# Kernel tuning notes

Hardware: AMD Instinct MI355X
Metric: run time of the kernel (lower is better)

## Reference

```python
import jax, jax.numpy as jnp
import numpy as np

N = 100000   # nodes
E = 3200000  # edges
G = 256      # graphs in batch
C_IN, H, OUT = 5, 64, 2
EPS = 1e-5


def setup_inputs() -> dict:
    key = jax.random.key(0)
    ks = jax.random.split(key, 16)
    d = {
        "x": jax.random.normal(ks[0], (N, C_IN), jnp.float32),
        "edge_index": jax.random.randint(ks[1], (2, E), 0, N, jnp.int64),
        "batch": jnp.sort(jax.random.randint(ks[2], (N,), 0, G, jnp.int64)),
        "W1": jax.random.normal(ks[3], (C_IN, H), jnp.float32),
        "b1": jax.random.normal(ks[4], (H,), jnp.float32),
        "g1": jax.random.uniform(ks[5], (H,), jnp.float32),
        "be1": jax.random.normal(ks[6], (H,), jnp.float32),
        "rm1": jnp.zeros((H,), jnp.float32),
        "rv1": jnp.ones((H,), jnp.float32),
        "W2": jax.random.normal(ks[7], (H, H), jnp.float32),
        "b2": jax.random.normal(ks[8], (H,), jnp.float32),
        "g2": jax.random.uniform(ks[9], (H,), jnp.float32),
        "be2": jax.random.normal(ks[10], (H,), jnp.float32),
        "rm2": jnp.zeros((H,), jnp.float32),
        "rv2": jnp.ones((H,), jnp.float32),
        "W3": jax.random.normal(ks[11], (H, H), jnp.float32),
        "b3": jax.random.normal(ks[12], (H,), jnp.float32),
        "g3": jax.random.uniform(ks[13], (H,), jnp.float32),
        "be3": jax.random.normal(ks[14], (H,), jnp.float32),
        "rm3": jnp.zeros((H,), jnp.float32),
        "rv3": jnp.ones((H,), jnp.float32),
        "Wf1": jax.random.normal(ks[15], (H, 32), jnp.float32),
        "bf1": jax.random.normal(jax.random.fold_in(key, 1), (32,), jnp.float32),
        "Wf2": jax.random.normal(jax.random.fold_in(key, 2), (32, OUT), jnp.float32),
        "bf2": jax.random.normal(jax.random.fold_in(key, 3), (OUT,), jnp.float32),
    }
    return d


def reference(x, edge_index, batch, W1, b1, g1, be1, rm1, rv1,
              W2, b2, g2, be2, rm2, rv2, W3, b3, g3, be3, rm3, rv3,
              Wf1, bf1, Wf2, bf2):
    src, dst = edge_index[0], edge_index[1]
    # GCN symmetric normalization with self-loops: deg includes the self edge
    deg = jax.ops.segment_sum(jnp.ones((E,), x.dtype), dst, num_segments=N) + 1.0
    dinv = jax.lax.rsqrt(deg)            # [N]
    enorm = dinv[src] * dinv[dst]        # per-edge norm  [E]
    snorm = dinv * dinv                  # self-loop norm [N]

    def gcn(h, W, b):
        h = h @ W                                                  # [N,H]
        agg = jax.ops.segment_sum(h[src] * enorm[:, None], dst, num_segments=N)
        return agg + h * snorm[:, None] + b

    def bn(h, g, be, rm, rv):  # eval-mode BatchNorm1d
        return (h - rm) * jax.lax.rsqrt(rv + EPS) * g + be

    h = jax.nn.relu(bn(gcn(x, W1, b1), g1, be1, rm1, rv1))
    h = jax.nn.relu(bn(gcn(h, W2, b2), g2, be2, rm2, rv2))
    h = jax.nn.relu(bn(gcn(h, W3, b3), g3, be3, rm3, rv3))

    counts = jax.ops.segment_sum(jnp.ones((N,), h.dtype), batch, num_segments=G)
    pooled = jax.ops.segment_sum(h, batch, num_segments=G) / jnp.maximum(counts, 1.0)[:, None]

    h = jax.nn.relu(pooled @ Wf1 + bf1)  # dropout is identity in eval
    return jax.nn.sigmoid(h @ Wf2 + bf2)
```

## Files before the change

### kernel.cpp

```cpp
#include <hip/hip_runtime.h>
#include <hip/hip_bf16.h>

#define HF 64
#define EPS 1e-5f

#define BSH 9
#define BKN (1 << BSH)
#define NBUCK_MAX 256
#define PB_T 256
#define PB_EPT 32
#define PB_TILE (PB_T * PB_EPT)

#define LGRID 2048

typedef __hip_bfloat16 bf16;

__device__ __forceinline__ unsigned char f32_to_fp8(float v) {
    int p = __builtin_amdgcn_cvt_pk_fp8_f32(v, v, 0, false);
    return (unsigned char)(p & 0xff);
}

__device__ __forceinline__ float rdlane(float v, int k) {
    return __int_as_float(__builtin_amdgcn_readlane(__float_as_int(v), k));
}

__device__ __forceinline__ unsigned bf16_rne_hi(float x) {
    unsigned u = __float_as_uint(x);
    return (u + 0x7fffu + ((u >> 16) & 1u)) & 0xffff0000u;
}

__global__ __launch_bounds__(PB_T) void k_passB2(
    const int* __restrict__ src, const int* __restrict__ dst,
    int* __restrict__ stage, unsigned* __restrict__ rtab,
    int* __restrict__ bcnt, int E, int B) {
    __shared__ int scnt[NBUCK_MAX];
    __shared__ int sscan[PB_T];
    int t = threadIdx.x;
    int blk = blockIdx.x;
    int tile0 = blk * PB_TILE;

    for (int b = t; b < NBUCK_MAX; b += PB_T) scnt[b] = 0;
    __syncthreads();

    int rec[PB_EPT];
    int bkt[PB_EPT];
#pragma unroll
    for (int k = 0; k < PB_EPT; ++k) {
        int e = tile0 + k * PB_T + t;
        bkt[k] = -1;
        if (e < E) {
            int d = dst[e];
            int s = src[e];
            int b = d >> BSH;
            bkt[k] = b;
            rec[k] = s | ((d & (BKN - 1)) << 17);
            atomicAdd(&scnt[b], 1);
        }
    }
    __syncthreads();

    int v = (t < B) ? scnt[t] : 0;
    sscan[t] = v;
    __syncthreads();
    for (int off = 1; off < PB_T; off <<= 1) {
        int val = sscan[t];
        int add = (t >= off) ? sscan[t - off] : 0;
        __syncthreads();
        sscan[t] = val + add;
        __syncthreads();
    }
    int excl = sscan[t] - v;
    if (t < B) {
        rtab[(size_t)blk * B + t] = ((unsigned)excl << 14) | (unsigned)v;
        scnt[t] = excl;
        if (v) atomicAdd(&bcnt[t], v);
    }
    __syncthreads();

#pragma unroll
    for (int k = 0; k < PB_EPT; ++k) {
        if (bkt[k] >= 0) {
            int loc = atomicAdd(&scnt[bkt[k]], 1);
            stage[tile0 + loc] = rec[k];
        }
    }
}

__global__ void k_bscan3(const int* __restrict__ bcnt, int* __restrict__ bbase2,
                         int* __restrict__ base, int B, int N, int E) {
    __shared__ int tot[NBUCK_MAX];
    int t = threadIdx.x;
    int v = (t < B) ? bcnt[t] : 0;
    tot[t] = v;
    __syncthreads();
    for (int off = 1; off < 256; off <<= 1) {
        int val = tot[t];
        int add = (t >= off) ? tot[t - off] : 0;
        __syncthreads();
        tot[t] = val + add;
        __syncthreads();
    }
    if (t < B) bbase2[t] = tot[t] - v;
    if (t == 0) { bbase2[B] = E; base[N] = E; }
}

__global__ __launch_bounds__(512) void k_passC2(const int* __restrict__ stage,
                                                const unsigned* __restrict__ rtab,
                                                const int* __restrict__ bb2,
                                                int* __restrict__ base,
                                                float* __restrict__ dinv,
                                                int* __restrict__ csr,
                                                int N, int B, int nblk) {
    __shared__ int lcnt[BKN];
    __shared__ int lscan[BKN];
    __shared__ int lcur[BKN];
    int beta = blockIdx.x;
    int n0 = beta * BKN;
    int n1 = n0 + BKN; if (n1 > N) n1 = N;
    int nn = n1 - n0;
    int t = threadIdx.x;
    int rg = t >> 4;
    int le = t & 15;
    lcnt[t] = 0;
    __syncthreads();

    for (int blk0 = 0; blk0 < nblk; blk0 += 32) {
        int blk = blk0 + rg;
        if (blk < nblk) {
            unsigned rt = rtab[(size_t)blk * B + beta];
            int cnt = (int)(rt & 0x3FFFu);
            int off = blk * PB_TILE + (int)(rt >> 14);
            for (int i = le; i < cnt; i += 16)
                atomicAdd(&lcnt[stage[off + i] >> 17], 1);
        }
    }
    __syncthreads();
    int v = lcnt[t];
    lscan[t] = v;
    __syncthreads();
    for (int off = 1; off < 512; off <<= 1) {
        int val = lscan[t];
        int add = (t >= off) ? lscan[t - off] : 0;
        __syncthreads();
        lscan[t] = val + add;
        __syncthreads();
    }
    int b = bb2[beta] + lscan[t] - v;
    if (t < nn) {
        base[n0 + t] = b;
        dinv[n0 + t] = rsqrtf((float)v + 1.0f);
    }
    lcur[t] = b;
    __syncthreads();

    for (int blk0 = 0; blk0 < nblk; blk0 += 32) {
        int blk = blk0 + rg;
        if (blk < nblk) {
            unsigned rt = rtab[(size_t)blk * B + beta];
            int cnt = (int)(rt & 0x3FFFu);
            int off = blk * PB_TILE + (int)(rt >> 14);
            for (int i = le; i < cnt; i += 16) {
                int r = stage[off + i];
                int pos = atomicAdd(&lcur[r >> 17], 1);
                csr[pos] = r & 0x1ffff;
            }
        }
    }
}

__global__ void k_prescale(const float* __restrict__ x, const float* __restrict__ dinv,
                           float* __restrict__ xs, int N5) {
    int i = blockIdx.x * blockDim.x + threadIdx.x;
    if (i < N5) xs[i] = x[i] * dinv[i / 5];
}

__global__ __launch_bounds__(256) void k_layer1(
    const float* __restrict__ xs, unsigned char* __restrict__ hout,
    const int* __restrict__ csr, const int* __restrict__ basep,
    const float* __restrict__ dinv,
    const float* __restrict__ W1, const float* __restrict__ b,
    const float* __restrict__ g, const float* __restrict__ be,
    const float* __restrict__ rm, const float* __restrict__ rv, int N) {
    __shared__ float sW[5 * HF];
    __shared__ float sB[HF];
    __shared__ float sScale[HF];
    if (threadIdx.x < HF) {
        int f = threadIdx.x;
        float scale = g[f] * rsqrtf(rv[f] + EPS);
        sScale[f] = scale;
        sB[f] = (b[f] - rm[f]) * scale + be[f];
    }
    __syncthreads();
    for (int i = threadIdx.x; i < 5 * HF; i += blockDim.x)
        sW[i] = W1[i] * sScale[i & (HF - 1)];
    __syncthreads();

    int lane = threadIdx.x & 63;
    int wave = threadIdx.x >> 6;
    int c  = lane & 7;
    int g8 = lane >> 3;
    int stride = gridDim.x * 4;

    auto mlp_store = [&](float accS, int nodeS, float diS) {
        float out = sB[lane];
#pragma unroll
        for (int k = 0; k < 5; ++k) out += __shfl(accS, k, 64) * sW[k * HF + lane];
        out = fmaxf(out, 0.f);
        hout[(size_t)nodeS * HF + lane] = f32_to_fp8(out * diS);
    };

    float accP = 0.f, diP = 0.f;
    int nodeP = -1;

    for (int node = blockIdx.x * 4 + wave; node < N; node += stride) {
        int j   = __builtin_amdgcn_readfirstlane(basep[node]);
        int end = __builtin_amdgcn_readfirstlane(basep[node + 1]);

        float a0 = 0.f, a1 = 0.f, a2 = 0.f, a3 = 0.f;
        if (g8 == 0 && c < 5) a0 = xs[node * 5 + c];

        float u0 = 0.f, u1 = 0.f, u2 = 0.f, u3 = 0.f;
        bool w0 = (j + 32 <= end);
        if (w0) {
            int s0 = csr[j + g8];
            int s1 = csr[j + 8 + g8];
            int s2 = csr[j + 16 + g8];
            int s3 = csr[j + 24 + g8];
            u0 = xs[s0 * 5 + c]; u1 = xs[s1 * 5 + c];
            u2 = xs[s2 * 5 + c]; u3 = xs[s3 * 5 + c];
        }

        if (nodeP >= 0) mlp_store(accP, nodeP, diP);

        if (w0) {
            j += 32;
            while (j + 32 <= end) {
                int s0 = csr[j + g8];
                int s1 = csr[j + 8 + g8];
                int s2 = csr[j + 16 + g8];
                int s3 = csr[j + 24 + g8];
                float v0 = xs[s0 * 5 + c];
                float v1 = xs[s1 * 5 + c];
                float v2 = xs[s2 * 5 + c];
                float v3 = xs[s3 * 5 + c];
                a0 += u0; a1 += u1; a2 += u2; a3 += u3;
                u0 = v0; u1 = v1; u2 = v2; u3 = v3;
                j += 32;
            }
            a0 += u0; a1 += u1; a2 += u2; a3 += u3;
        }
        for (; j + 8 <= end; j += 8) {
            int s = csr[j + g8];
            a0 += xs[s * 5 + c];
        }
        if (j < end && j + g8 < end) {
            int s = csr[j + g8];
            a0 += xs[s * 5 + c];
        }

        float acc = (a0 + a1) + (a2 + a3);
        acc += __shfl_xor(acc, 8, 64);
        acc += __shfl_xor(acc, 16, 64);
        acc += __shfl_xor(acc, 32, 64);

        float di = dinv[node];
        accP = acc * di;
        diP = di;
        nodeP = node;
    }
    if (nodeP >= 0) mlp_store(accP, nodeP, diP);
}

template <int SCALE_OUT>
__global__ __launch_bounds__(256, 4) void k_layer(
    const unsigned char* __restrict__ hs8, void* __restrict__ hout_v,
    const int* __restrict__ csr, const int* __restrict__ basep,
    const float* __restrict__ dinv,
    const float* __restrict__ W, const float* __restrict__ b,
    const float* __restrict__ g, const float* __restrict__ be,
    const float* __restrict__ rm, const float* __restrict__ rv, int N) {
    __shared__ uint4 swp4[64][9];

    int lane = threadIdx.x & 63;
    int wave = threadIdx.x >> 6;
    int stride = gridDim.x * 4;
    const unsigned char* col = hs8 + lane;

    if (threadIdx.x < 64) {
        int l = threadIdx.x;
        float sc = g[l] * rsqrtf(rv[l] + EPS);
#pragma unroll
        for (int c = 0; c < 8; ++c) {
            unsigned p[4];
#pragma unroll
            for (int q = 0; q < 4; ++q) {
                int k2 = c * 4 + q;
                unsigned lo = bf16_rne_hi(W[(2 * k2 + 0) * HF + l] * sc);
                unsigned hi = bf16_rne_hi(W[(2 * k2 + 1) * HF + l] * sc);
                p[q] = (lo >> 16) | hi;
            }
            swp4[l][c] = make_uint4(p[0], p[1], p[2], p[3]);
        }
    }
    __syncthreads();

    float scale = g[lane] * rsqrtf(rv[lane] + EPS);
    float bias  = (b[lane] - rm[lane]) * scale + be[lane];

    auto mlp_store = [&](float acc, int nodeS, float diS) {
        float o0 = bias, o1 = 0.f, o2 = 0.f, o3 = 0.f;
#pragma unroll
        for (int c = 0; c < 8; ++c) {
            uint4 pv = swp4[lane][c];
            int k0 = c * 8;
            o0 += rdlane(acc, k0 + 0) * __uint_as_float(pv.x << 16);
            o1 += rdlane(acc, k0 + 1) * __uint_as_float(pv.x & 0xffff0000u);
            o2 += rdlane(acc, k0 + 2) * __uint_as_float(pv.y << 16);
            o3 += rdlane(acc, k0 + 3) * __uint_as_float(pv.y & 0xffff0000u);
            o0 += rdlane(acc, k0 + 4) * __uint_as_float(pv.z << 16);
            o1 += rdlane(acc, k0 + 5) * __uint_as_float(pv.z & 0xffff0000u);
            o2 += rdlane(acc, k0 + 6) * __uint_as_float(pv.w << 16);
            o3 += rdlane(acc, k0 + 7) * __uint_as_float(pv.w & 0xffff0000u);
        }
        float out = fmaxf((o0 + o1) + (o2 + o3), 0.f);
        if (SCALE_OUT) {
            ((unsigned char*)hout_v)[(size_t)nodeS * HF + lane] = f32_to_fp8(out * diS);
        } else {
            ((float*)hout_v)[(size_t)nodeS * HF + lane] = out;
        }
    };

    float accP = 0.f, diP = 0.f;
    int nodeP = -1;

    for (int node = blockIdx.x * 4 + wave; node < N; node += stride) {
        int j   = __builtin_amdgcn_readfirstlane(basep[node]);
        int end = __builtin_amdgcn_readfirstlane(basep[node + 1]);

        float a0 = __builtin_amdgcn_cvt_f32_fp8((unsigned)col[(size_t)node * HF], 0);
        float a1 = 0.f, a2 = 0.f, a3 = 0.f;

        unsigned u0 = 0, u1 = 0, u2 = 0, u3 = 0, u4 = 0, u5 = 0, u6 = 0, u7 = 0;
        bool w0 = (j + 8 <= end);
        if (w0) {
            int s0 = csr[j+0], s1 = csr[j+1], s2 = csr[j+2], s3 = csr[j+3];
            int s4 = csr[j+4], s5 = csr[j+5], s6 = csr[j+6], s7 = csr[j+7];
            u0 = col[(size_t)s0 * HF]; u1 = col[(size_t)s1 * HF];
            u2 = col[(size_t)s2 * HF]; u3 = col[(size_t)s3 * HF];
            u4 = col[(size_t)s4 * HF]; u5 = col[(size_t)s5 * HF];
            u6 = col[(size_t)s6 * HF]; u7 = col[(size_t)s7 * HF];
        }

        if (nodeP >= 0) mlp_store(accP, nodeP, diP);

        if (w0) {
            j += 8;
            while (j + 8 <= end) {
                int t0 = csr[j+0], t1 = csr[j+1], t2 = csr[j+2], t3 = csr[j+3];
                int t4 = csr[j+4], t5 = csr[j+5], t6 = csr[j+6], t7 = csr[j+7];
                unsigned v0 = col[(size_t)t0 * HF];
                unsigned v1 = col[(size_t)t1 * HF];
                unsigned v2 = col[(size_t)t2 * HF];
                unsigned v3 = col[(size_t)t3 * HF];
                unsigned v4 = col[(size_t)t4 * HF];
                unsigned v5 = col[(size_t)t5 * HF];
                unsigned v6 = col[(size_t)t6 * HF];
                unsigned v7 = col[(size_t)t7 * HF];
                a0 += __builtin_amdgcn_cvt_f32_fp8(u0, 0);
                a1 += __builtin_amdgcn_cvt_f32_fp8(u1, 0);
                a2 += __builtin_amdgcn_cvt_f32_fp8(u2, 0);
                a3 += __builtin_amdgcn_cvt_f32_fp8(u3, 0);
                a0 += __builtin_amdgcn_cvt_f32_fp8(u4, 0);
                a1 += __builtin_amdgcn_cvt_f32_fp8(u5, 0);
                a2 += __builtin_amdgcn_cvt_f32_fp8(u6, 0);
                a3 += __builtin_amdgcn_cvt_f32_fp8(u7, 0);
                u0 = v0; u1 = v1; u2 = v2; u3 = v3;
                u4 = v4; u5 = v5; u6 = v6; u7 = v7;
                j += 8;
            }
            a0 += __builtin_amdgcn_cvt_f32_fp8(u0, 0);
            a1 += __builtin_amdgcn_cvt_f32_fp8(u1, 0);
            a2 += __builtin_amdgcn_cvt_f32_fp8(u2, 0);
            a3 += __builtin_amdgcn_cvt_f32_fp8(u3, 0);
            a0 += __builtin_amdgcn_cvt_f32_fp8(u4, 0);
            a1 += __builtin_amdgcn_cvt_f32_fp8(u5, 0);
            a2 += __builtin_amdgcn_cvt_f32_fp8(u6, 0);
            a3 += __builtin_amdgcn_cvt_f32_fp8(u7, 0);
        }
        for (; j < end; ++j) {
            int s = csr[j];
            a0 += __builtin_amdgcn_cvt_f32_fp8((unsigned)col[(size_t)s * HF], 0);
        }

        float di = dinv[node];
        accP = ((a0 + a1) + (a2 + a3)) * di;
        diP = di;
        nodeP = node;
    }
    if (nodeP >= 0) mlp_store(accP, nodeP, diP);
}

__global__ void k_pool_fc(const float* __restrict__ h, const int* __restrict__ batch,
                          const float* __restrict__ Wf1, const float* __restrict__ bf1,
                          const float* __restrict__ Wf2, const float* __restrict__ bf2,
                          float* __restrict__ out, int N) {
    int g = blockIdx.x;
    int t = threadIdx.x;
    int f = t & 63, q = t >> 6;

    int lo = 0, hi = N;
    while (lo < hi) { int mid = (lo + hi) >> 1; if (batch[mid] < g) lo = mid + 1; else hi = mid; }
    int start = lo;
    hi = N;
    while (lo < hi) { int mid = (lo + hi) >> 1; if (batch[mid] < g + 1) lo = mid + 1; else hi = mid; }
    int end = lo;

    float sum = 0.f;
    for (int n = start + q; n < end; n += 4) sum += h[n * HF + f];

    __shared__ float red[4][HF];
    __shared__ float sp[HF];
    __shared__ float sh[32];
    red[q][f] = sum;
    __syncthreads();
    if (q == 0) {
        float s = red[0][f] + red[1][f] + red[2][f] + red[3][f];
        float cntf = (float)(end - start);
        sp[f] = s / fmaxf(cntf, 1.0f);
    }
    __syncthreads();
    if (t < 32) {
        float a = bf1[t];
#pragma unroll
        for (int k = 0; k < HF; ++k) a += sp[k] * Wf1[k * 32 + t];
        sh[t] = fmaxf(a, 0.f);
    }
    __syncthreads();
    if (t < 2) {
        float a = bf2[t];
#pragma unroll
        for (int k = 0; k < 32; ++k) a += sh[k] * Wf2[k * 2 + t];
        out[g * 2 + t] = 1.f / (1.f + expf(-a));
    }
}

extern "C" void kernel_launch(void* const* d_in, const int* in_sizes, int n_in,
                              void* d_out, int out_size, void* d_ws, size_t ws_size,
                              hipStream_t stream) {
    const float* x     = (const float*)d_in[0];
    const int*   ei    = (const int*)d_in[1];
    const int*   batch = (const int*)d_in[2];
    const float* W1 = (const float*)d_in[3];
    const float* b1 = (const float*)d_in[4];
    const float* g1 = (const float*)d_in[5];
    const float* be1 = (const float*)d_in[6];
    const float* rm1 = (const float*)d_in[7];
    const float* rv1 = (const float*)d_in[8];
    const float* W2 = (const float*)d_in[9];
    const float* b2 = (const float*)d_in[10];
    const float* g2 = (const float*)d_in[11];
    const float* be2 = (const float*)d_in[12];
    const float* rm2 = (const float*)d_in[13];
    const float* rv2 = (const float*)d_in[14];
    const float* W3 = (const float*)d_in[15];
    const float* b3 = (const float*)d_in[16];
    const float* g3 = (const float*)d_in[17];
    const float* be3 = (const float*)d_in[18];
    const float* rm3 = (const float*)d_in[19];
    const float* rv3 = (const float*)d_in[20];
    const float* Wf1 = (const float*)d_in[21];
    const float* bf1 = (const float*)d_in[22];
    const float* Wf2 = (const float*)d_in[23];
    const float* bf2 = (const float*)d_in[24];
    float* out = (float*)d_out;

    const int N = in_sizes[2];
    const int E = in_sizes[1] / 2;
    const int G = out_size / 2;
    const int B = (N + BKN - 1) / BKN;

    char* ws = (char*)d_ws;
    size_t off = 0;
    auto alloc = [&](size_t bytes) {
        char* p = ws + off;
        off += (bytes + 255) & ~(size_t)255;
        return p;
    };
    const int nblk = (E + PB_TILE - 1) / PB_TILE;

    float*         H3       = (float*)alloc((size_t)N * HF * sizeof(float));
    unsigned char* HS1      = (unsigned char*)alloc((size_t)N * HF);
    unsigned char* HS2      = (unsigned char*)alloc((size_t)N * HF);
    float*         xs       = (float*)alloc((size_t)N * 5 * sizeof(float) + 64);
    float*         dinv     = (float*)alloc((size_t)N * sizeof(float));
    int*           base     = (int*)  alloc(((size_t)N + 1) * sizeof(int));
    int*           bcnt     = (int*)  alloc((size_t)NBUCK_MAX * sizeof(int));
    int*           bbase2   = (int*)  alloc(((size_t)NBUCK_MAX + 1) * sizeof(int));
    unsigned*      rtab     = (unsigned*)alloc((size_t)nblk * B * sizeof(unsigned));
    int*           csr      = (int*)  alloc((size_t)E * sizeof(int));
    int*           stage    = (int*)H3;

    const int* src = ei;
    const int* dst = ei + E;

    const int BT = 256;
    int gP  = (N * 5 + BT - 1) / BT;

    hipMemsetAsync(bcnt, 0, (size_t)B * sizeof(int), stream);
    k_passB2<<<nblk, PB_T, 0, stream>>>(src, dst, stage, rtab, bcnt, E, B);
    k_bscan3<<<1, 256, 0, stream>>>(bcnt, bbase2, base, B, N, E);
    k_passC2<<<B, 512, 0, stream>>>(stage, rtab, bbase2, base, dinv, csr, N, B, nblk);
    k_prescale<<<gP, BT, 0, stream>>>(x, dinv, xs, N * 5);

    k_layer1<<<LGRID, BT, 0, stream>>>(xs, HS1, csr, base, dinv,
                                       W1, b1, g1, be1, rm1, rv1, N);
    k_layer<1><<<LGRID, BT, 0, stream>>>(HS1, HS2, csr, base, dinv,
                                         W2, b2, g2, be2, rm2, rv2, N);
    k_layer<0><<<LGRID, BT, 0, stream>>>(HS2, H3, csr, base, dinv,
                                         W3, b3, g3, be3, rm3, rv3, N);

    k_pool_fc<<<G, BT, 0, stream>>>(H3, batch, Wf1, bf1, Wf2, bf2, out, N);
}
```

Before: 419.5 us.

## Use fp16 dot2 for the fused MLP, bf16 final activations, and deeper gather unrolling

The per-node 64x64 matmul now packs weights and activations to fp16 and uses packed dot2 instructions instead of scalar bf16-decoded FMAs. The last layer's output is stored as bf16 rather than fp32, and the pooling kernel reads it back as bf16, which halves that buffer's traffic. The neighbour gather loop is unrolled to 16 loads in flight with an 8-wide tail, and the grid size for the layer kernels is raised. These trade extra numerical error from fp16/bf16 rounding and higher register pressure for fewer ALU ops and more memory-level parallelism.

```diff
diff --git a/kernel.cpp b/kernel.cpp
--- a/kernel.cpp
+++ b/kernel.cpp
@@ -11,9 +11,16 @@
 #define PB_EPT 32
 #define PB_TILE (PB_T * PB_EPT)
 
-#define LGRID 2048
+#define LGRID 3072
 
 typedef __hip_bfloat16 bf16;
+typedef __fp16 f16x2 __attribute__((ext_vector_type(2)));
+
+#if __has_builtin(__builtin_amdgcn_fdot2) && __has_builtin(__builtin_amdgcn_cvt_pkrtz)
+#define USE_FDOT2 1
+#else
+#define USE_FDOT2 0
+#endif
 
 __device__ __forceinline__ unsigned char f32_to_fp8(float v) {
     int p = __builtin_amdgcn_cvt_pk_fp8_f32(v, v, 0, false);
@@ -28,6 +35,16 @@
     unsigned u = __float_as_uint(x);
     return (u + 0x7fffu + ((u >> 16) & 1u)) & 0xffff0000u;
 }
+
+#if USE_FDOT2
+__device__ __forceinline__ unsigned pack_f16(float a, float b) {
+    f16x2 h = __builtin_amdgcn_cvt_pkrtz(a, b);
+    union { f16x2 h; unsigned u; } c; c.h = h; return c.u;
+}
+__device__ __forceinline__ f16x2 as_f16x2(unsigned u) {
+    union { unsigned u; f16x2 h; } c; c.u = u; return c.h;
+}
+#endif
 
 __global__ __launch_bounds__(PB_T) void k_passB2(
     const int* __restrict__ src, const int* __restrict__ dst,
@@ -295,9 +312,13 @@
 #pragma unroll
             for (int q = 0; q < 4; ++q) {
                 int k2 = c * 4 + q;
-                unsigned lo = bf16_rne_hi(W[(2 * k2 + 0) * HF + l] * sc);
-                unsigned hi = bf16_rne_hi(W[(2 * k2 + 1) * HF + l] * sc);
-                p[q] = (lo >> 16) | hi;
+                float w0 = W[(2 * k2 + 0) * HF + l] * sc;
+                float w1 = W[(2 * k2 + 1) * HF + l] * sc;
+#if USE_FDOT2
+                p[q] = pack_f16(w0, w1);
+#else
+                p[q] = (bf16_rne_hi(w0) >> 16) | bf16_rne_hi(w1);
+#endif
             }
             swp4[l][c] = make_uint4(p[0], p[1], p[2], p[3]);
         }
@@ -313,20 +334,32 @@
         for (int c = 0; c < 8; ++c) {
             uint4 pv = swp4[lane][c];
             int k0 = c * 8;
+#if USE_FDOT2
+            f16x2 a01 = __builtin_amdgcn_cvt_pkrtz(rdlane(acc, k0 + 0), rdlane(acc, k0 + 1));
+            f16x2 a23 = __builtin_amdgcn_cvt_pkrtz(rdlane(acc, k0 + 2), rdlane(acc, k0 + 3));
+            f16x2 a45 = __builtin_amdgcn_cvt_pkrtz(rdlane(acc, k0 + 4), rdlane(acc, k0 + 5));
+            f16x2 a67 = __builtin_amdgcn_cvt_pkrtz(rdlane(acc, k0 + 6), rdlane(acc, k0 + 7));
+            o0 = __builtin_amdgcn_fdot2(a01, as_f16x2(pv.x), o0, false);
+            o1 = __builtin_amdgcn_fdot2(a23, as_f16x2(pv.y), o1, false);
+            o2 = __builtin_amdgcn_fdot2(a45, as_f16x2(pv.z), o2, false);
+            o3 = __builtin_amdgcn_fdot2(a67, as_f16x2(pv.w), o3, false);
+#else
             o0 += rdlane(acc, k0 + 0) * __uint_as_float(pv.x << 16);
             o1 += rdlane(acc, k0 + 1) * __uint_as_float(pv.x & 0xffff0000u);
-            o2 += rdlane(acc, k0 + 2) * __uint_as_float(pv.y << 16);
-            o3 += rdlane(acc, k0 + 3) * __uint_as_float(pv.y & 0xffff0000u);
-            o0 += rdlane(acc, k0 + 4) * __uint_as_float(pv.z << 16);
-            o1 += rdlane(acc, k0 + 5) * __uint_as_float(pv.z & 0xffff0000u);
+            o0 += rdlane(acc, k0 + 2) * __uint_as_float(pv.y << 16);
+            o1 += rdlane(acc, k0 + 3) * __uint_as_float(pv.y & 0xffff0000u);
+            o2 += rdlane(acc, k0 + 4) * __uint_as_float(pv.z << 16);
+            o3 += rdlane(acc, k0 + 5) * __uint_as_float(pv.z & 0xffff0000u);
             o2 += rdlane(acc, k0 + 6) * __uint_as_float(pv.w << 16);
             o3 += rdlane(acc, k0 + 7) * __uint_as_float(pv.w & 0xffff0000u);
+#endif
         }
         float out = fmaxf((o0 + o1) + (o2 + o3), 0.f);
         if (SCALE_OUT) {
             ((unsigned char*)hout_v)[(size_t)nodeS * HF + lane] = f32_to_fp8(out * diS);
         } else {
-            ((float*)hout_v)[(size_t)nodeS * HF + lane] = out;
+            ((unsigned short*)hout_v)[(size_t)nodeS * HF + lane] =
+                (unsigned short)(bf16_rne_hi(out) >> 16);
         }
     };
 
@@ -341,31 +374,40 @@
         float a1 = 0.f, a2 = 0.f, a3 = 0.f;
 
         unsigned u0 = 0, u1 = 0, u2 = 0, u3 = 0, u4 = 0, u5 = 0, u6 = 0, u7 = 0;
-        bool w0 = (j + 8 <= end);
+        unsigned u8 = 0, u9 = 0, uA = 0, uB = 0, uC = 0, uD = 0, uE = 0, uF = 0;
+        bool w0 = (j + 16 <= end);
         if (w0) {
-            int s0 = csr[j+0], s1 = csr[j+1], s2 = csr[j+2], s3 = csr[j+3];
-            int s4 = csr[j+4], s5 = csr[j+5], s6 = csr[j+6], s7 = csr[j+7];
+            int s0 = csr[j+0],  s1 = csr[j+1],  s2 = csr[j+2],  s3 = csr[j+3];
+            int s4 = csr[j+4],  s5 = csr[j+5],  s6 = csr[j+6],  s7 = csr[j+7];
+            int s8 = csr[j+8],  s9 = csr[j+9],  sA = csr[j+10], sB_ = csr[j+11];
+            int sC = csr[j+12], sD = csr[j+13], sE = csr[j+14], sF = csr[j+15];
             u0 = col[(size_t)s0 * HF]; u1 = col[(size_t)s1 * HF];
             u2 = col[(size_t)s2 * HF]; u3 = col[(size_t)s3 * HF];
             u4 = col[(size_t)s4 * HF]; u5 = col[(size_t)s5 * HF];
             u6 = col[(size_t)s6 * HF]; u7 = col[(size_t)s7 * HF];
+            u8 = col[(size_t)s8 * HF]; u9 = col[(size_t)s9 * HF];
+            uA = col[(size_t)sA * HF]; uB = col[(size_t)sB_ * HF];
+            uC = col[(size_t)sC * HF]; uD = col[(size_t)sD * HF];
+            uE = col[(size_t)sE * HF]; uF = col[(size_t)sF * HF];
         }
 
         if (nodeP >= 0) mlp_store(accP, nodeP, diP);
 
         if (w0) {
-            j += 8;
-            while (j + 8 <= end) {
-                int t0 = csr[j+0], t1 = csr[j+1], t2 = csr[j+2], t3 = csr[j+3];
-                int t4 = csr[j+4], t5 = csr[j+5], t6 = csr[j+6], t7 = csr[j+7];
-                unsigned v0 = col[(size_t)t0 * HF];
-                unsigned v1 = col[(size_t)t1 * HF];
-                unsigned v2 = col[(size_t)t2 * HF];
-                unsigned v3 = col[(size_t)t3 * HF];
-                unsigned v4 = col[(size_t)t4 * HF];
-                unsigned v5 = col[(size_t)t5 * HF];
-                unsigned v6 = col[(size_t)t6 * HF];
-                unsigned v7 = col[(size_t)t7 * HF];
+            j += 16;
+            while (j + 16 <= end) {
+                int t0 = csr[j+0],  t1 = csr[j+1],  t2 = csr[j+2],  t3 = csr[j+3];
+                int t4 = csr[j+4],  t5 = csr[j+5],  t6 = csr[j+6],  t7 = csr[j+7];
+                int t8 = csr[j+8],  t9 = csr[j+9],  tA = csr[j+10], tB = csr[j+11];
+                int tC = csr[j+12], tD = csr[j+13], tE = csr[j+14], tF = csr[j+15];
+                unsigned v0 = col[(size_t)t0 * HF], v1 = col[(size_t)t1 * HF];
+                unsigned v2 = col[(size_t)t2 * HF], v3 = col[(size_t)t3 * HF];
+                unsigned v4 = col[(size_t)t4 * HF], v5 = col[(size_t)t5 * HF];
+                unsigned v6 = col[(size_t)t6 * HF], v7 = col[(size_t)t7 * HF];
+                unsigned v8 = col[(size_t)t8 * HF], v9 = col[(size_t)t9 * HF];
+                unsigned vA = col[(size_t)tA * HF], vB = col[(size_t)tB * HF];
+                unsigned vC = col[(size_t)tC * HF], vD = col[(size_t)tD * HF];
+                unsigned vE = col[(size_t)tE * HF], vF = col[(size_t)tF * HF];
                 a0 += __builtin_amdgcn_cvt_f32_fp8(u0, 0);
                 a1 += __builtin_amdgcn_cvt_f32_fp8(u1, 0);
                 a2 += __builtin_amdgcn_cvt_f32_fp8(u2, 0);
@@ -374,9 +416,19 @@
                 a1 += __builtin_amdgcn_cvt_f32_fp8(u5, 0);
                 a2 += __builtin_amdgcn_cvt_f32_fp8(u6, 0);
                 a3 += __builtin_amdgcn_cvt_f32_fp8(u7, 0);
+                a0 += __builtin_amdgcn_cvt_f32_fp8(u8, 0);
+                a1 += __builtin_amdgcn_cvt_f32_fp8(u9, 0);
+                a2 += __builtin_amdgcn_cvt_f32_fp8(uA, 0);
+                a3 += __builtin_amdgcn_cvt_f32_fp8(uB, 0);
+                a0 += __builtin_amdgcn_cvt_f32_fp8(uC, 0);
+                a1 += __builtin_amdgcn_cvt_f32_fp8(uD, 0);
+                a2 += __builtin_amdgcn_cvt_f32_fp8(uE, 0);
+                a3 += __builtin_amdgcn_cvt_f32_fp8(uF, 0);
                 u0 = v0; u1 = v1; u2 = v2; u3 = v3;
                 u4 = v4; u5 = v5; u6 = v6; u7 = v7;
-                j += 8;
+                u8 = v8; u9 = v9; uA = vA; uB = vB;
+                uC = vC; uD = vD; uE = vE; uF = vF;
+                j += 16;
             }
             a0 += __builtin_amdgcn_cvt_f32_fp8(u0, 0);
             a1 += __builtin_amdgcn_cvt_f32_fp8(u1, 0);
@@ -386,6 +438,30 @@
             a1 += __builtin_amdgcn_cvt_f32_fp8(u5, 0);
             a2 += __builtin_amdgcn_cvt_f32_fp8(u6, 0);
             a3 += __builtin_amdgcn_cvt_f32_fp8(u7, 0);
+            a0 += __builtin_amdgcn_cvt_f32_fp8(u8, 0);
+            a1 += __builtin_amdgcn_cvt_f32_fp8(u9, 0);
+            a2 += __builtin_amdgcn_cvt_f32_fp8(uA, 0);
+            a3 += __builtin_amdgcn_cvt_f32_fp8(uB, 0);
+            a0 += __builtin_amdgcn_cvt_f32_fp8(uC, 0);
+            a1 += __builtin_amdgcn_cvt_f32_fp8(uD, 0);
+            a2 += __builtin_amdgcn_cvt_f32_fp8(uE, 0);
+            a3 += __builtin_amdgcn_cvt_f32_fp8(uF, 0);
+        }
+        for (; j + 8 <= end; j += 8) {
+            int s0 = csr[j+0], s1 = csr[j+1], s2 = csr[j+2], s3 = csr[j+3];
+            int s4 = csr[j+4], s5 = csr[j+5], s6 = csr[j+6], s7 = csr[j+7];
+            unsigned w0_ = col[(size_t)s0 * HF], w1_ = col[(size_t)s1 * HF];
+            unsigned w2_ = col[(size_t)s2 * HF], w3_ = col[(size_t)s3 * HF];
+            unsigned w4_ = col[(size_t)s4 * HF], w5_ = col[(size_t)s5 * HF];
+            unsigned w6_ = col[(size_t)s6 * HF], w7_ = col[(size_t)s7 * HF];
+            a0 += __builtin_amdgcn_cvt_f32_fp8(w0_, 0);
+            a1 += __builtin_amdgcn_cvt_f32_fp8(w1_, 0);
+            a2 += __builtin_amdgcn_cvt_f32_fp8(w2_, 0);
+            a3 += __builtin_amdgcn_cvt_f32_fp8(w3_, 0);
+            a0 += __builtin_amdgcn_cvt_f32_fp8(w4_, 0);
+            a1 += __builtin_amdgcn_cvt_f32_fp8(w5_, 0);
+            a2 += __builtin_amdgcn_cvt_f32_fp8(w6_, 0);
+            a3 += __builtin_amdgcn_cvt_f32_fp8(w7_, 0);
         }
         for (; j < end; ++j) {
             int s = csr[j];
@@ -400,7 +476,7 @@
     if (nodeP >= 0) mlp_store(accP, nodeP, diP);
 }
 
-__global__ void k_pool_fc(const float* __restrict__ h, const int* __restrict__ batch,
+__global__ void k_pool_fc(const unsigned short* __restrict__ h, const int* __restrict__ batch,
                           const float* __restrict__ Wf1, const float* __restrict__ bf1,
                           const float* __restrict__ Wf2, const float* __restrict__ bf2,
                           float* __restrict__ out, int N) {
@@ -416,7 +492,8 @@
     int end = lo;
 
     float sum = 0.f;
-    for (int n = start + q; n < end; n += 4) sum += h[n * HF + f];
+    for (int n = start + q; n < end; n += 4)
+        sum += __uint_as_float(((unsigned)h[(size_t)n * HF + f]) << 16);
 
     __shared__ float red[4][HF];
     __shared__ float sp[HF];
@@ -488,7 +565,9 @@
     };
     const int nblk = (E + PB_TILE - 1) / PB_TILE;
 
-    float*         H3       = (float*)alloc((size_t)N * HF * sizeof(float));
+    size_t h3_bytes = (size_t)N * HF * 2;
+    size_t st_bytes = (size_t)E * 4;
+    unsigned short* H3 = (unsigned short*)alloc(h3_bytes > st_bytes ? h3_bytes : st_bytes);
     unsigned char* HS1      = (unsigned char*)alloc((size_t)N * HF);
     unsigned char* HS2      = (unsigned char*)alloc((size_t)N * HF);
     float*         xs       = (float*)alloc((size_t)N * 5 * sizeof(float) + 64);
```

New measurement: 435.2 us. 1.04x slower.
